# Kernel optimization log

Measured on AMD Instinct MI355X. Metric: run time of the kernel, lower is better.

The kernel has to match this reference:

```python
import jax, jax.numpy as jnp
import numpy as np
import math

B, TQ, TK, D, H, K = 4, 1024, 1536, 1024, 16, 1
DV = D // H * K  # 64
DP = D * K       # projection dim


def setup_inputs() -> dict:
    key = jax.random.key(0)
    ks = jax.random.split(key, 12)
    s = 0.02
    query = jax.random.normal(ks[0], (B, TQ, D), dtype=jnp.float32)
    key_value = jax.random.normal(ks[1], (B, TK, D), dtype=jnp.float32)
    relative = jax.random.normal(ks[2], (B, TK, D), dtype=jnp.float32)
    # Transformer-XL causal mask: query i may attend to key j <= i + mem
    mem = TK - TQ
    i = jnp.arange(TQ)[:, None]
    j = jnp.arange(TK)[None, :]
    mask = jnp.broadcast_to(j > i + mem, (B, TQ, TK))  # True = masked
    Wq = jax.random.normal(ks[3], (D, DP), dtype=jnp.float32) * s
    Wk = jax.random.normal(ks[4], (D, DP), dtype=jnp.float32) * s
    Wv = jax.random.normal(ks[5], (D, DP), dtype=jnp.float32) * s
    Wr = jax.random.normal(ks[6], (D, DP), dtype=jnp.float32) * s
    Wo = jax.random.normal(ks[7], (DP, D), dtype=jnp.float32) * s
    u = jax.random.normal(ks[8], (DV,), dtype=jnp.float32) * s
    v = jax.random.normal(ks[9], (DV,), dtype=jnp.float32) * s
    gamma = jnp.ones((D,), dtype=jnp.float32)
    beta = jnp.zeros((D,), dtype=jnp.float32)
    return {"query": query, "key_value": key_value, "relative": relative,
            "mask": mask, "Wq": Wq, "Wk": Wk, "Wv": Wv, "Wr": Wr, "Wo": Wo,
            "u": u, "v": v, "gamma": gamma, "beta": beta}


def _layer_norm(x, gamma, beta, eps=1e-5):
    mu = jnp.mean(x, axis=-1, keepdims=True)
    var = jnp.mean(jnp.square(x - mu), axis=-1, keepdims=True)
    return (x - mu) * jax.lax.rsqrt(var + eps) * gamma + beta


def reference(query, key_value, relative, mask, Wq, Wk, Wv, Wr, Wo, u, v, gamma, beta):
    b, tq, d = query.shape
    tk = key_value.shape[1]
    dv = u.shape[0]
    h = Wq.shape[1] // dv
    q = (query @ Wq).reshape(b, tq, h, dv)
    k = (key_value @ Wk).reshape(b, tk, h, dv)
    val = (key_value @ Wv).reshape(b, tk, h, dv)
    r = (relative @ Wr).reshape(b, tk, h, dv)
    # content term (q+u)K^T and position term (q+v)R^T, per head
    ac = jnp.einsum('bqhd,bkhd->bhqk', q + u, k)
    bd = jnp.einsum('bqhd,bkhd->bhqk', q + v, r)
    logits = (ac + bd) * (1.0 / math.sqrt(dv))
    logits = jnp.where(mask[:, None, :, :], -jnp.inf, logits)
    w = jax.nn.softmax(logits, axis=-1)
    ctx = jnp.einsum('bhqk,bkhd->bqhd', w, val).reshape(b, tq, h * dv)
    out = ctx @ Wo + query  # residual
    return _layer_norm(out, gamma, beta)
```

## Files before the change

### kernel.cpp

```cpp
#include <hip/hip_runtime.h>


typedef unsigned short u16;
typedef __attribute__((ext_vector_type(8))) short short8;
typedef __attribute__((ext_vector_type(4))) float floatx4;

__device__ __forceinline__ float bf2f(u16 u) {
    union { unsigned int i; float f; } w; w.i = ((unsigned int)u) << 16; return w.f;
}
__device__ __forceinline__ u16 f2bf(float f) {
    union { unsigned int i; float f; } w; w.f = f;
    unsigned int u = w.i;
    return (u16)((u + 0x7FFFu + ((u >> 16) & 1u)) >> 16);
}

__device__ __forceinline__ void gl_lds16(const u16* g, u16* lds) {
    __builtin_amdgcn_global_load_lds(
        (const __attribute__((address_space(1))) void*)g,
        (__attribute__((address_space(3))) void*)lds, 16, 0, 0);
}

__global__ __launch_bounds__(256) void cvt3_kernel(
    const float* __restrict__ x0, u16* __restrict__ y0, int n0,
    const float* __restrict__ x1, u16* __restrict__ y1, int n1,
    const float* __restrict__ x2, u16* __restrict__ y2, int n2)
{
    const int which = blockIdx.y;
    const float* x = (which == 0) ? x0 : (which == 1) ? x1 : x2;
    u16* y         = (which == 0) ? y0 : (which == 1) ? y1 : y2;
    const int n    = (which == 0) ? n0 : (which == 1) ? n1 : n2;
    const int i = (blockIdx.x * 256 + threadIdx.x) * 8;
    if (i >= n) return;
    float4 a = *(const float4*)&x[i];
    float4 b = *(const float4*)&x[i + 4];
    short8 o;
    o[0] = (short)f2bf(a.x); o[1] = (short)f2bf(a.y);
    o[2] = (short)f2bf(a.z); o[3] = (short)f2bf(a.w);
    o[4] = (short)f2bf(b.x); o[5] = (short)f2bf(b.y);
    o[6] = (short)f2bf(b.z); o[7] = (short)f2bf(b.w);
    *(short8*)&y[i] = o;
}

__global__ __launch_bounds__(256) void transpose5_kernel(
    const float* __restrict__ Wq, const float* __restrict__ Wk,
    const float* __restrict__ Wr, const float* __restrict__ Wv,
    const float* __restrict__ Wo,
    u16* __restrict__ WqT, u16* __restrict__ WkrT,
    u16* __restrict__ WvT, u16* __restrict__ WoT)
{
    const int z = blockIdx.z;
    const float* W; u16* WT; int dst_ld, dst_koff;
    switch (z) {
        case 0: W = Wq; WT = WqT;  dst_ld = 1024; dst_koff = 0;    break;
        case 1: W = Wk; WT = WkrT; dst_ld = 2048; dst_koff = 0;    break;
        case 2: W = Wr; WT = WkrT; dst_ld = 2048; dst_koff = 1024; break;
        case 3: W = Wv; WT = WvT;  dst_ld = 1024; dst_koff = 0;    break;
        default:W = Wo; WT = WoT;  dst_ld = 1024; dst_koff = 0;    break;
    }
    __shared__ u16 ts[64][72];
    const int k0 = blockIdx.x * 64, n0 = blockIdx.y * 64;
    const int r  = threadIdx.x >> 2;
    const int c4 = (threadIdx.x & 3) << 4;
    const float* src = &W[(size_t)(k0 + r) * 1024 + n0 + c4];
    for (int j = 0; j < 16; j += 4) {
        float4 a = *(const float4*)(src + j);
        ts[r][c4 + j + 0] = f2bf(a.x);
        ts[r][c4 + j + 1] = f2bf(a.y);
        ts[r][c4 + j + 2] = f2bf(a.z);
        ts[r][c4 + j + 3] = f2bf(a.w);
    }
    __syncthreads();
    short8 t0, t1;
    for (int j = 0; j < 8; j++) t0[j] = (short)ts[c4 + j][r];
    for (int j = 0; j < 8; j++) t1[j] = (short)ts[c4 + 8 + j][r];
    u16* dst = &WT[(size_t)(n0 + r) * dst_ld + dst_koff + k0 + c4];
    *(short8*)dst       = t0;
    *(short8*)(dst + 8) = t1;
}

__global__ __launch_bounds__(256) void wuv_kernel(
    const float* __restrict__ Wk, const float* __restrict__ Wr,
    const float* __restrict__ u, const float* __restrict__ v,
    u16* __restrict__ wuvb)
{
    int idx = blockIdx.x * 256 + threadIdx.x;
    int c = idx >> 4, h = idx & 15;
    float au = 0.f, av = 0.f;
    for (int d = 0; d < 64; d++) {
        au += Wk[(size_t)c * 1024 + h * 64 + d] * u[d];
        av += Wr[(size_t)c * 1024 + h * 64 + d] * v[d];
    }
    wuvb[h * 2048 + c]        = f2bf(au);
    wuvb[h * 2048 + 1024 + c] = f2bf(av);
}

template <int EPI>
__device__ __forceinline__ void gemm_body(
    const u16* __restrict__ A0, const u16* __restrict__ A1,
    const u16* __restrict__ WT, void* __restrict__ out,
    int Kld, int kbeg, int kend, int Ksplit, int T,
    int bm, int bn, u16* As, u16* Ws)
{
    const int tid = threadIdx.x;
    const int wave = tid >> 6, lane = tid & 63;
    const int wm = wave >> 1, wn = wave & 1;
    const int l16 = lane & 15, quad = lane >> 4;

    floatx4 acc[4][4];
    const floatx4 zf = {0.f, 0.f, 0.f, 0.f};
    for (int i = 0; i < 4; i++) for (int j = 0; j < 4; j++) acc[i][j] = zf;

    const int m_base = bm * 128, n_base = bn * 128;
    const int rl = lane >> 2;
    const int cl = (lane & 3) * 8;

    for (int k0 = kbeg; k0 < kend; k0 += 32) {
        const u16* Aptr; int kk;
        if (k0 < Ksplit) { Aptr = A0; kk = k0; } else { Aptr = A1; kk = k0 - Ksplit; }
        __syncthreads();
        for (int half = 0; half < 2; half++) {
            const int r = wave * 32 + half * 16;
            gl_lds16(Aptr + (size_t)(m_base + r + rl) * 1024 + kk + cl, &As[r * 32]);
            gl_lds16(WT   + (size_t)(n_base + r + rl) * Kld  + k0 + cl, &Ws[r * 32]);
        }
        __syncthreads();

        short8 af[4], bf[4];
        for (int i = 0; i < 4; i++) {
            af[i] = *(const short8*)&As[(wm * 64 + i * 16 + l16) * 32 + quad * 8];
            bf[i] = *(const short8*)&Ws[(wn * 64 + i * 16 + l16) * 32 + quad * 8];
        }
        for (int i = 0; i < 4; i++)
            for (int j = 0; j < 4; j++)
                acc[i][j] = __builtin_amdgcn_mfma_f32_16x16x32_bf16(af[i], bf[j], acc[i][j], 0, 0, 0);
    }

    for (int i = 0; i < 4; i++) {
        for (int rg = 0; rg < 4; rg++) {
            const int m = m_base + wm * 64 + i * 16 + quad * 4 + rg;
            if (EPI == 0) {
                const int b = m / T, t = m % T;
                u16* op = (u16*)out;
                for (int j = 0; j < 4; j++) {
                    const int col = n_base + wn * 64 + j * 16 + l16;
                    const int h = col >> 6, d = col & 63;
                    op[((((size_t)b * 16 + h) * T + t) << 6) + d] = f2bf(acc[i][j][rg]);
                }
            } else if (EPI == 2) {
                const int b = m / T, t = m % T;
                u16* op = (u16*)out;
                for (int j = 0; j < 4; j++) {
                    const int col = n_base + wn * 64 + j * 16 + l16;
                    const int h = col >> 6, d = col & 63;
                    op[(((size_t)b * 16 + h) * 64 + d) * 1536 + t] = f2bf(acc[i][j][rg]);
                }
            } else {
                float* op = (float*)out;
                for (int j = 0; j < 4; j++) {
                    const int col = n_base + wn * 64 + j * 16 + l16;
                    op[(size_t)m * 1024 + col] = acc[i][j][rg];
                }
            }
        }
    }
}

__device__ __forceinline__ void bias_body(
    const u16* __restrict__ kvb, const u16* __restrict__ relb,
    const u16* __restrict__ wuvb, float* __restrict__ bias, int bblk)
{
    const int tid = threadIdx.x;
    const int wave = tid >> 6, lane = tid & 63;
    const int l16 = lane & 15, quad = lane >> 4;
    const int tBase = bblk * 64 + wave * 16;

    floatx4 acc = {0.f, 0.f, 0.f, 0.f};
    const u16* arow_kv  = kvb  + (size_t)(tBase + l16) * 1024;
    const u16* arow_rel = relb + (size_t)(tBase + l16) * 1024;
    const u16* brow     = wuvb + (size_t)l16 * 2048;

    for (int ks = 0; ks < 64; ks++) {
        const int k0 = ks * 32;
        const u16* ap = (k0 < 1024) ? (arow_kv + k0) : (arow_rel + k0 - 1024);
        short8 af = *(const short8*)(ap + quad * 8);
        short8 bf = *(const short8*)(brow + k0 + quad * 8);
        acc = __builtin_amdgcn_mfma_f32_16x16x32_bf16(af, bf, acc, 0, 0, 0);
    }
    for (int rg = 0; rg < 4; rg++) {
        const int tg = tBase + quad * 4 + rg;
        const int b = tg / 1536, t = tg % 1536;
        bias[((size_t)b * 16 + l16) * 1536 + t] = acc[rg];
    }
}

__global__ __launch_bounds__(256) void fused_proj(
    const u16* __restrict__ qb, const u16* __restrict__ kvb,
    const u16* __restrict__ relb,
    const u16* __restrict__ WqT, const u16* __restrict__ WkrT,
    const u16* __restrict__ WvT, const u16* __restrict__ wuvb,
    u16* __restrict__ Qh, u16* __restrict__ KRh, u16* __restrict__ Vt,
    float* __restrict__ bias)
{
    __shared__ u16 smem[2 * 128 * 32];
    u16* As = smem;
    u16* Ws = smem + 128 * 32;
    const int blk = blockIdx.x;
    if (blk < 384) {
        gemm_body<0>(kvb, relb, WkrT, KRh, 2048, 0, 2048, 1024, 1536,
                     blk % 48, blk / 48, As, Ws);
    } else if (blk < 768) {
        const int i = blk - 384;
        gemm_body<2>(kvb, nullptr, WvT, Vt, 1024, 0, 1024, 1024, 1536,
                     i % 48, i / 48, As, Ws);
    } else if (blk < 1024) {
        const int i = blk - 768;
        gemm_body<0>(qb, nullptr, WqT, Qh, 1024, 0, 1024, 1024, 1024,
                     i % 32, i / 32, As, Ws);
    } else {
        bias_body(kvb, relb, wuvb, bias, blk - 1024);
    }
}

__global__ __launch_bounds__(256) void out_gemm(
    const u16* __restrict__ ctx, const u16* __restrict__ WoT,
    float* __restrict__ outp)
{
    __shared__ u16 smem[2 * 128 * 32];
    const int z = blockIdx.z;
    gemm_body<3>(ctx, nullptr, WoT,
                 outp + (size_t)z * 4 * 1024 * 1024, 1024,
                 z * 512, z * 512 + 512, 1024, 1024,
                 blockIdx.x, blockIdx.y, smem, smem + 128 * 32);
}

__global__ __launch_bounds__(256) void attn_kernel(
    const u16* __restrict__ Qh,
    const u16* __restrict__ KRh,
    const u16* __restrict__ Vt,
    const float* __restrict__ bias,
    u16* __restrict__ ctx)
{
    const int blk  = blockIdx.x;
    const int hb   = blk & 63;
    const int qblk = blk >> 6;
    const int b = hb >> 4, h = hb & 15;
    const int tid = threadIdx.x;
    const int wave = tid >> 6, lane = tid & 63;
    const int l16 = lane & 15, quad = lane >> 4;
    const int q0 = qblk * 128;

    const u16* Qp = Qh  + (size_t)hb * 1024 * 64;
    const u16* Kp = KRh + (size_t)hb * 1536 * 64;
    const u16* Vp = Vt  + (size_t)hb * 64 * 1536;
    const float* bp = bias + (size_t)hb * 1536;

    __shared__ u16 Ps[4][2][16][68];

    short8 aq[2][2];
    for (int mi = 0; mi < 2; mi++)
        for (int ks = 0; ks < 2; ks++)
            aq[mi][ks] = *(const short8*)
                &Qp[(size_t)(q0 + wave * 32 + mi * 16 + l16) * 64 + ks * 32 + quad * 8];

    const floatx4 zf = {0.f, 0.f, 0.f, 0.f};
    floatx4 accO[2][4];
    float lsum[2][4];
    for (int mi = 0; mi < 2; mi++)
        for (int j = 0; j < 4; j++) accO[mi][j] = zf;
    for (int mi = 0; mi < 2; mi++)
        for (int rg = 0; rg < 4; rg++) lsum[mi][rg] = 0.f;

    const int nkt = 2 * qblk + 10;
    for (int kt = 0; kt < nkt; kt++) {
        const int k0 = kt * 64;

        short8 bk[4][2], bv[4][2];
        float bcol[4];
        for (int n = 0; n < 4; n++)
            for (int ks = 0; ks < 2; ks++)
                bk[n][ks] = *(const short8*)
                    &Kp[(size_t)(k0 + n * 16 + l16) * 64 + ks * 32 + quad * 8];
        for (int j = 0; j < 4; j++)
            for (int ks = 0; ks < 2; ks++)
                bv[j][ks] = *(const short8*)
                    &Vp[(size_t)(j * 16 + l16) * 1536 + k0 + ks * 32 + quad * 8];
        for (int n = 0; n < 4; n++) bcol[n] = bp[k0 + n * 16 + l16];

        const bool domask = (k0 + 63 > q0 + 512);

        for (int mi = 0; mi < 2; mi++) {
            floatx4 accS[4];
            for (int n = 0; n < 4; n++) {
                accS[n] = zf;
                for (int ks = 0; ks < 2; ks++)
                    accS[n] = __builtin_amdgcn_mfma_f32_16x16x32_bf16(
                        aq[mi][ks], bk[n][ks], accS[n], 0, 0, 0);
            }
            const int qrow = q0 + wave * 32 + mi * 16 + quad * 4;
            for (int n = 0; n < 4; n++) {
                const int col = k0 + n * 16 + l16;
                for (int rg = 0; rg < 4; rg++) {
                    float s = (accS[n][rg] + bcol[n]) * 0.125f;
                    if (domask && col > qrow + rg + 512) s = -1e30f;
                    const float p = __expf(s);
                    lsum[mi][rg] += p;
                    Ps[wave][mi][quad * 4 + rg][n * 16 + l16] = f2bf(p);
                }
            }
            short8 ap[2];
            for (int ks = 0; ks < 2; ks++)
                ap[ks] = *(const short8*)&Ps[wave][mi][l16][ks * 32 + quad * 8];
            for (int j = 0; j < 4; j++)
                for (int ks = 0; ks < 2; ks++)
                    accO[mi][j] = __builtin_amdgcn_mfma_f32_16x16x32_bf16(
                        ap[ks], bv[j][ks], accO[mi][j], 0, 0, 0);
        }
    }

    for (int mi = 0; mi < 2; mi++)
        for (int rg = 0; rg < 4; rg++) {
            float s = lsum[mi][rg];
            for (int off = 1; off < 16; off <<= 1) s += __shfl_xor(s, off, 64);
            lsum[mi][rg] = s;
        }

    for (int mi = 0; mi < 2; mi++)
        for (int j = 0; j < 4; j++)
            for (int rg = 0; rg < 4; rg++) {
                const int q = q0 + wave * 32 + mi * 16 + quad * 4 + rg;
                const int d = j * 16 + l16;
                ctx[((size_t)b * 1024 + q) * 1024 + h * 64 + d] =
                    f2bf(accO[mi][j][rg] / lsum[mi][rg]);
            }
}

__global__ __launch_bounds__(256) void ln_kernel(
    const float* __restrict__ x0, const float* __restrict__ x1,
    const float* __restrict__ q,
    const float* __restrict__ gamma, const float* __restrict__ beta,
    float* __restrict__ out)
{
    const int row = blockIdx.x;
    const int tid = threadIdx.x;
    const size_t base = (size_t)row * 1024 + tid * 4;
    float4 a = *(const float4*)&x0[base];
    float4 c = *(const float4*)&x1[base];
    float4 r = *(const float4*)&q[base];
    float4 v;
    v.x = a.x + c.x + r.x; v.y = a.y + c.y + r.y;
    v.z = a.z + c.z + r.z; v.w = a.w + c.w + r.w;
    float s  = v.x + v.y + v.z + v.w;
    float ss = v.x * v.x + v.y * v.y + v.z * v.z + v.w * v.w;
    for (int off = 1; off < 64; off <<= 1) {
        s  += __shfl_xor(s, off, 64);
        ss += __shfl_xor(ss, off, 64);
    }
    __shared__ float sm[8];
    const int wave = tid >> 6, lane = tid & 63;
    if (lane == 0) { sm[wave] = s; sm[4 + wave] = ss; }
    __syncthreads();
    s  = sm[0] + sm[1] + sm[2] + sm[3];
    ss = sm[4] + sm[5] + sm[6] + sm[7];
    const float mu  = s * (1.f / 1024.f);
    const float var = ss * (1.f / 1024.f) - mu * mu;
    const float inv = rsqrtf(var + 1e-5f);
    float* op = out + (size_t)row * 1024;
    const float* ve = &v.x;
    for (int j = 0; j < 4; j++) {
        const int c2 = tid * 4 + j;
        op[c2] = (ve[j] - mu) * inv * gamma[c2] + beta[c2];
    }
}

extern "C" void kernel_launch(void* const* d_in, const int* in_sizes, int n_in,
                              void* d_out, int out_size, void* d_ws, size_t ws_size,
                              hipStream_t stream)
{
    const float* query     = (const float*)d_in[0];
    const float* key_value = (const float*)d_in[1];
    const float* relative  = (const float*)d_in[2];
    const float* Wq = (const float*)d_in[4];
    const float* Wk = (const float*)d_in[5];
    const float* Wv = (const float*)d_in[6];
    const float* Wr = (const float*)d_in[7];
    const float* Wo = (const float*)d_in[8];
    const float* u  = (const float*)d_in[9];
    const float* v  = (const float*)d_in[10];
    const float* gamma = (const float*)d_in[11];
    const float* beta  = (const float*)d_in[12];

    char* wsp = (char*)d_ws;
    auto alloc = [&](size_t bytes) -> char* {
        char* p = wsp; wsp += (bytes + 255) & ~(size_t)255; return p;
    };
    u16*   qb   = (u16*)alloc((size_t)4 * 1024 * 1024 * 2);
    u16*   kvb  = (u16*)alloc((size_t)4 * 1536 * 1024 * 2);
    u16*   relb = (u16*)alloc((size_t)4 * 1536 * 1024 * 2);
    u16*   WqT  = (u16*)alloc((size_t)1024 * 1024 * 2);
    u16*   WkrT = (u16*)alloc((size_t)1024 * 2048 * 2);
    u16*   WvT  = (u16*)alloc((size_t)1024 * 1024 * 2);
    u16*   WoT  = (u16*)alloc((size_t)1024 * 1024 * 2);
    u16*   wuvb = (u16*)alloc((size_t)16 * 2048 * 2);
    u16*   Qh   = (u16*)alloc((size_t)4 * 16 * 1024 * 64 * 2);
    u16*   KRh  = (u16*)alloc((size_t)4 * 16 * 1536 * 64 * 2);
    u16*   Vt   = (u16*)alloc((size_t)4 * 16 * 64 * 1536 * 2);
    float* bias = (float*)alloc((size_t)4 * 16 * 1536 * 4);
    u16*   ctx  = (u16*)alloc((size_t)4 * 1024 * 1024 * 2);
    float* outp = (float*)alloc((size_t)2 * 4 * 1024 * 1024 * 4);

    const dim3 tb(256);
    cvt3_kernel<<<dim3(3072, 3), tb, 0, stream>>>(
        query, qb, 4 * 1024 * 1024,
        key_value, kvb, 4 * 1536 * 1024,
        relative, relb, 4 * 1536 * 1024);

    transpose5_kernel<<<dim3(16, 16, 5), tb, 0, stream>>>(
        Wq, Wk, Wr, Wv, Wo, WqT, WkrT, WvT, WoT);
    wuv_kernel<<<64, tb, 0, stream>>>(Wk, Wr, u, v, wuvb);

    fused_proj<<<dim3(1120), tb, 0, stream>>>(
        qb, kvb, relb, WqT, WkrT, WvT, wuvb, Qh, KRh, Vt, bias);

    attn_kernel<<<dim3(512), tb, 0, stream>>>(Qh, KRh, Vt, bias, ctx);

    out_gemm<<<dim3(32, 8, 2), tb, 0, stream>>>(ctx, WoT, outp);
    ln_kernel<<<4096, tb, 0, stream>>>(
        outp, outp + (size_t)4 * 1024 * 1024, query, gamma, beta, (float*)d_out);
}
```

Measured before the change: 346.5 us.

## Rewrite projection GEMMs as 256x256 tiles with 512 threads and pipelined LDS staging

The fused projection kernel moves from 128x128 tiles on 256 threads to 256x256 tiles on 512 threads. LDS staging is now a 4-slot ring buffer that loads two k-steps ahead, with an XOR swizzle against bank conflicts, phase-split barriers and s_setprio around the MFMA bursts. The aim is more reuse per loaded byte and better overlap of global loads with matrix math. Bias blocks now cover 128 rows each. The cost is far fewer blocks (304 vs 1120), so the 256 CUs may be less evenly loaded, plus higher register and LDS pressure.

```diff
diff --git a/kernel.cpp b/kernel.cpp
--- a/kernel.cpp
+++ b/kernel.cpp
@@ -138,41 +138,150 @@
     for (int i = 0; i < 4; i++) {
         for (int rg = 0; rg < 4; rg++) {
             const int m = m_base + wm * 64 + i * 16 + quad * 4 + rg;
-            if (EPI == 0) {
-                const int b = m / T, t = m % T;
-                u16* op = (u16*)out;
-                for (int j = 0; j < 4; j++) {
-                    const int col = n_base + wn * 64 + j * 16 + l16;
-                    const int h = col >> 6, d = col & 63;
-                    op[((((size_t)b * 16 + h) * T + t) << 6) + d] = f2bf(acc[i][j][rg]);
+            float* op = (float*)out;
+            for (int j = 0; j < 4; j++) {
+                const int col = n_base + wn * 64 + j * 16 + l16;
+                op[(size_t)m * 1024 + col] = acc[i][j][rg];
+            }
+        }
+    }
+}
+
+__device__ __forceinline__ void stage_half(
+    const u16* __restrict__ src, int src_ld, int row_base, int col_base,
+    u16* lds_slot, int wave, int lane)
+{
+    const int r = wave * 16 + (lane >> 2);
+    const int c = (((lane & 3) ^ ((lane >> 2) & 3)) << 3);
+    gl_lds16(src + (size_t)(row_base + r) * src_ld + col_base + c,
+             lds_slot + wave * 512);
+    gl_lds16(src + (size_t)(row_base + 128 + r) * src_ld + col_base + c,
+             lds_slot + 4096 + wave * 512);
+}
+
+template <int EPI, int T>
+__device__ __forceinline__ void gemm256_body(
+    const u16* __restrict__ A0, const u16* __restrict__ A1,
+    const u16* __restrict__ WT, void* __restrict__ out,
+    int Kld, int NT, int KsplitTile, int bm, int bn,
+    u16* As, u16* Bs)
+{
+    const int tid  = threadIdx.x;
+    const int wave = tid >> 6, lane = tid & 63;
+    const int wm = wave >> 2, wn = wave & 3;
+    const int l16 = lane & 15, quad = lane >> 4;
+    const int m_base = bm * 256, n_base = bn * 256;
+
+    floatx4 acc[8][4];
+    const floatx4 zf = {0.f, 0.f, 0.f, 0.f};
+    #pragma unroll
+    for (int i = 0; i < 8; i++)
+        #pragma unroll
+        for (int j = 0; j < 4; j++) acc[i][j] = zf;
+
+    {
+        const u16* sa0 = (0 < KsplitTile) ? A0 : A1;
+        stage_half(sa0, 1024, m_base, 0,  As + 0 * 8192, wave, lane);
+        stage_half(WT,  Kld,  n_base, 0,  Bs + 0 * 8192, wave, lane);
+        stage_half(sa0, 1024, m_base, 32, As + 1 * 8192, wave, lane);
+        stage_half(WT,  Kld,  n_base, 32, Bs + 1 * 8192, wave, lane);
+        const u16* sa1 = (1 < KsplitTile) ? A0 : A1;
+        const int  c1  = (1 < KsplitTile) ? 64 : (1 - KsplitTile) * 64;
+        stage_half(sa1, 1024, m_base, c1, As + 2 * 8192, wave, lane);
+        stage_half(WT,  Kld,  n_base, 64, Bs + 2 * 8192, wave, lane);
+    }
+
+    for (int t = 0; t < NT; ++t) {
+        if (t + 1 < NT) asm volatile("s_waitcnt vmcnt(4)" ::: "memory");
+        else            asm volatile("s_waitcnt vmcnt(0)" ::: "memory");
+        __builtin_amdgcn_s_barrier();
+
+        short8 bfr[4];
+        #pragma unroll
+        for (int ph = 0; ph < 4; ++ph) {
+            if (ph) __builtin_amdgcn_s_barrier();
+            const int ks = ph >> 1, mh = ph & 1;
+
+            if (ph == 0) {
+                if (t + 1 < NT) {
+                    const int tt = t + 1;
+                    const u16* sa = (tt < KsplitTile) ? A0 : A1;
+                    const int cb = (tt < KsplitTile ? tt : tt - KsplitTile) * 64 + 32;
+                    stage_half(sa, 1024, m_base, cb, As + ((2 * tt + 1) & 3) * 8192, wave, lane);
                 }
-            } else if (EPI == 2) {
-                const int b = m / T, t = m % T;
-                u16* op = (u16*)out;
-                for (int j = 0; j < 4; j++) {
-                    const int col = n_base + wn * 64 + j * 16 + l16;
-                    const int h = col >> 6, d = col & 63;
-                    op[(((size_t)b * 16 + h) * 64 + d) * 1536 + t] = f2bf(acc[i][j][rg]);
+            } else if (ph == 1) {
+                if (t + 1 < NT)
+                    stage_half(WT, Kld, n_base, (t + 1) * 64 + 32,
+                               Bs + ((2 * (t + 1) + 1) & 3) * 8192, wave, lane);
+            } else if (ph == 2) {
+                if (t + 2 < NT) {
+                    const int tt = t + 2;
+                    const u16* sa = (tt < KsplitTile) ? A0 : A1;
+                    const int cb = (tt < KsplitTile ? tt : tt - KsplitTile) * 64;
+                    stage_half(sa, 1024, m_base, cb, As + ((2 * tt) & 3) * 8192, wave, lane);
                 }
             } else {
-                float* op = (float*)out;
-                for (int j = 0; j < 4; j++) {
-                    const int col = n_base + wn * 64 + j * 16 + l16;
-                    op[(size_t)m * 1024 + col] = acc[i][j][rg];
+                if (t + 2 < NT)
+                    stage_half(WT, Kld, n_base, (t + 2) * 64,
+                               Bs + ((2 * (t + 2)) & 3) * 8192, wave, lane);
+            }
+
+            const u16* Aslot = As + ((2 * t + ks) & 3) * 8192;
+            const u16* Bslot = Bs + ((2 * t + ks) & 3) * 8192;
+            if (mh == 0) {
+                #pragma unroll
+                for (int nj = 0; nj < 4; ++nj) {
+                    const int row = wn * 64 + nj * 16 + l16;
+                    bfr[nj] = *(const short8*)&Bslot[row * 32 + (((quad ^ row) & 3) << 3)];
                 }
             }
-        }
-    }
-}
-
-__device__ __forceinline__ void bias_body(
+            short8 af[4];
+            #pragma unroll
+            for (int mi = 0; mi < 4; ++mi) {
+                const int row = wm * 128 + mh * 64 + mi * 16 + l16;
+                af[mi] = *(const short8*)&Aslot[row * 32 + (((quad ^ row) & 3) << 3)];
+            }
+
+            __builtin_amdgcn_s_setprio(1);
+            #pragma unroll
+            for (int mi = 0; mi < 4; ++mi)
+                #pragma unroll
+                for (int nj = 0; nj < 4; ++nj)
+                    acc[mh * 4 + mi][nj] = __builtin_amdgcn_mfma_f32_16x16x32_bf16(
+                        af[mi], bfr[nj], acc[mh * 4 + mi][nj], 0, 0, 0);
+            __builtin_amdgcn_s_setprio(0);
+        }
+    }
+
+    u16* op = (u16*)out;
+    #pragma unroll
+    for (int mi = 0; mi < 8; ++mi) {
+        #pragma unroll
+        for (int rg = 0; rg < 4; ++rg) {
+            const int m = m_base + wm * 128 + mi * 16 + quad * 4 + rg;
+            const int b = m / T, tk = m % T;
+            #pragma unroll
+            for (int nj = 0; nj < 4; ++nj) {
+                const int col = n_base + wn * 64 + nj * 16 + l16;
+                const int h = col >> 6, d = col & 63;
+                if (EPI == 0) {
+                    op[(((size_t)(b * 16 + h) * T + tk) << 6) + d] = f2bf(acc[mi][nj][rg]);
+                } else {
+                    op[((size_t)(b * 16 + h) * 64 + d) * 1536 + tk] = f2bf(acc[mi][nj][rg]);
+                }
+            }
+        }
+    }
+}
+
+__device__ __forceinline__ void bias_body8(
     const u16* __restrict__ kvb, const u16* __restrict__ relb,
     const u16* __restrict__ wuvb, float* __restrict__ bias, int bblk)
 {
     const int tid = threadIdx.x;
     const int wave = tid >> 6, lane = tid & 63;
     const int l16 = lane & 15, quad = lane >> 4;
-    const int tBase = bblk * 64 + wave * 16;
+    const int tBase = bblk * 128 + wave * 16;
 
     floatx4 acc = {0.f, 0.f, 0.f, 0.f};
     const u16* arow_kv  = kvb  + (size_t)(tBase + l16) * 1024;
@@ -193,7 +302,7 @@
     }
 }
 
-__global__ __launch_bounds__(256) void fused_proj(
+__global__ __launch_bounds__(512) void fused_proj_v2(
     const u16* __restrict__ qb, const u16* __restrict__ kvb,
     const u16* __restrict__ relb,
     const u16* __restrict__ WqT, const u16* __restrict__ WkrT,
@@ -201,23 +310,22 @@
     u16* __restrict__ Qh, u16* __restrict__ KRh, u16* __restrict__ Vt,
     float* __restrict__ bias)
 {
-    __shared__ u16 smem[2 * 128 * 32];
-    u16* As = smem;
-    u16* Ws = smem + 128 * 32;
+    __shared__ __align__(128) u16 As[4 * 256 * 32];
+    __shared__ __align__(128) u16 Bs[4 * 256 * 32];
     const int blk = blockIdx.x;
-    if (blk < 384) {
-        gemm_body<0>(kvb, relb, WkrT, KRh, 2048, 0, 2048, 1024, 1536,
-                     blk % 48, blk / 48, As, Ws);
-    } else if (blk < 768) {
-        const int i = blk - 384;
-        gemm_body<2>(kvb, nullptr, WvT, Vt, 1024, 0, 1024, 1024, 1536,
-                     i % 48, i / 48, As, Ws);
-    } else if (blk < 1024) {
-        const int i = blk - 768;
-        gemm_body<0>(qb, nullptr, WqT, Qh, 1024, 0, 1024, 1024, 1024,
-                     i % 32, i / 32, As, Ws);
+    if (blk < 96) {
+        gemm256_body<0, 1536>(kvb, relb, WkrT, KRh, 2048, 32, 16,
+                              blk % 24, blk / 24, As, Bs);
+    } else if (blk < 192) {
+        const int i = blk - 96;
+        gemm256_body<2, 1536>(kvb, kvb, WvT, Vt, 1024, 16, 99,
+                              i % 24, i / 24, As, Bs);
+    } else if (blk < 256) {
+        const int i = blk - 192;
+        gemm256_body<0, 1024>(qb, qb, WqT, Qh, 1024, 16, 99,
+                              i % 16, i / 16, As, Bs);
     } else {
-        bias_body(kvb, relb, wuvb, bias, blk - 1024);
+        bias_body8(kvb, relb, wuvb, bias, blk - 256);
     }
 }
 
@@ -418,7 +526,7 @@
         Wq, Wk, Wr, Wv, Wo, WqT, WkrT, WvT, WoT);
     wuv_kernel<<<64, tb, 0, stream>>>(Wk, Wr, u, v, wuvb);
 
-    fused_proj<<<dim3(1120), tb, 0, stream>>>(
+    fused_proj_v2<<<dim3(304), dim3(512), 0, stream>>>(
         qb, kvb, relb, WqT, WkrT, WvT, wuvb, Qh, KRh, Vt, bias);
 
     attn_kernel<<<dim3(512), tb, 0, stream>>>(Qh, KRh, Vt, bias, ctx);
```

Result: faster. 336.6 us (-2.9%).
